# Optimization experiments

Measured on AMD Instinct MI355X. Metric: run time of the kernel, lower is better.

The kernel has to match this reference:

```python
import jax, jax.numpy as jnp
import numpy as np
from jax import lax

B, N, C, D = 8, 512, 37, 2048          # frames, rois/frame, classes (incl. bg), feat dim
SCORE_THR = 0.1
NMS_THR = 0.4
BBOX_STDS = np.array([0.1, 0.1, 0.2, 0.2], dtype=np.float32)


def setup_inputs() -> dict:
    key = jax.random.key(0)
    k1, k2, k3, k4, k5, k6 = jax.random.split(key, 6)
    # rois: [batch_idx, x1, y1, x2, y2] in a 600x1000 image
    x1 = jax.random.uniform(k1, (B, N)) * 900.0
    y1 = jax.random.uniform(k2, (B, N)) * 500.0
    w = jax.random.uniform(k3, (B, N)) * 120.0 + 8.0
    h = jax.random.uniform(k4, (B, N)) * 120.0 + 8.0
    bidx = jnp.broadcast_to(jnp.arange(B, dtype=jnp.float32)[:, None], (B, N))
    rois = jnp.stack([bidx, x1, y1, x1 + w, y1 + h], axis=-1)  # [B,N,5]
    bbox_pred = jax.random.normal(k5, (B, N, 4 * C)) * 0.5
    scores = jax.nn.softmax(jax.random.normal(k6, (B, N, C)) * 2.0, axis=-1)
    im_info = jnp.tile(jnp.array([[600.0, 1000.0, 1.0]], dtype=jnp.float32), (B, 1))
    roi_features = jax.random.normal(jax.random.fold_in(key, 7), (B, N, D))
    return {"rois": rois, "bbox_pred": bbox_pred, "scores": scores,
            "im_info": im_info, "roi_features": roi_features}


def _iou_matrix(b):
    # b: [N,4] -> [N,N] pairwise IoU (torchvision nms convention, no +1)
    area = (b[:, 2] - b[:, 0]) * (b[:, 3] - b[:, 1])
    lt = jnp.maximum(b[:, None, :2], b[None, :, :2])
    rb = jnp.minimum(b[:, None, 2:], b[None, :, 2:])
    wh = jnp.clip(rb - lt, 0.0)
    inter = wh[..., 0] * wh[..., 1]
    return inter / (area[:, None] + area[None, :] - inter + 1e-9)


def _nms_one(boxes, scores):
    # boxes [N,4], scores [N] -> keep mask [N] (greedy NMS on score-thresholded boxes)
    n = boxes.shape[0]
    valid = scores > SCORE_THR
    order = jnp.argsort(-jnp.where(valid, scores, -jnp.inf))
    b = boxes[order]
    v = valid[order]
    iou = _iou_matrix(b)
    idx = jnp.arange(n)

    def body(i, keep):
        suppressed = jnp.any((iou[:, i] > NMS_THR) & keep & (idx < i))
        return keep.at[i].set(v[i] & ~suppressed)

    keep_sorted = lax.fori_loop(0, n, body, jnp.zeros(n, bool))
    return jnp.zeros(n, bool).at[order].set(keep_sorted)


def reference(rois, bbox_pred, scores, im_info, roi_features):
    stds = jnp.asarray(BBOX_STDS)
    deltas = bbox_pred.reshape(B, N, C, 4) * stds
    # bbox_transform_inv
    w = (rois[..., 3] - rois[..., 1])[..., None]             # [B,N,1]
    h = (rois[..., 4] - rois[..., 2])[..., None]
    cx = rois[..., 1][..., None] + 0.5 * w
    cy = rois[..., 2][..., None] + 0.5 * h
    px = deltas[..., 0] * w + cx
    py = deltas[..., 1] * h + cy
    pw = jnp.exp(deltas[..., 2]) * w
    ph = jnp.exp(deltas[..., 3]) * h
    x1 = px - 0.5 * pw
    y1 = py - 0.5 * ph
    x2 = px + 0.5 * pw
    y2 = py + 0.5 * ph
    # clip_boxes to image
    xmax = (im_info[:, 1] - 1.0)[:, None, None]
    ymax = (im_info[:, 0] - 1.0)[:, None, None]
    boxes = jnp.stack([jnp.clip(x1, 0.0, xmax), jnp.clip(y1, 0.0, ymax),
                       jnp.clip(x2, 0.0, xmax), jnp.clip(y2, 0.0, ymax)], axis=-1)  # [B,N,C,4]
    # foreground classes 1..C-1, class-major layout: [B,C-1,N,*]
    boxes_fg = jnp.moveaxis(boxes[:, :, 1:, :], 2, 1)        # [B,C-1,N,4]
    scores_fg = jnp.moveaxis(scores[:, :, 1:], 2, 1)         # [B,C-1,N]
    keep = jax.vmap(jax.vmap(_nms_one))(boxes_fg, scores_fg)  # [B,C-1,N] bool
    cls_dets = jnp.where(keep[..., None],
                         jnp.concatenate([boxes_fg, scores_fg[..., None]], axis=-1),
                         0.0)                                 # [B,C-1,N,5]
    kept_feats = jnp.where(jnp.any(keep, axis=1)[..., None], roi_features, 0.0)  # [B,N,D]
    return cls_dets, kept_feats, keep
```

## Files before the change

### kernel.cpp

```cpp
#include <hip/hip_runtime.h>
#include <math.h>

#define BATCH 8
#define BN    512
#define NC    37
#define NFG   36
#define FD    2048


__global__ __launch_bounds__(64) void nms_kernel(
    const float* __restrict__ rois,
    const float* __restrict__ bbox_pred,
    const float* __restrict__ scores,
    const float* __restrict__ im_info,
    float* __restrict__ cls_dets,
    float* __restrict__ keep_out)
{
    const int bc   = blockIdx.x;
    const int b    = bc / NFG;
    const int cc   = bc % NFG;
    const int c    = cc + 1;
    const int lane = threadIdx.x;

    __shared__ float sb[BN][4];
    __shared__ float sarea[BN];
    __shared__ float cscore[BN];
    __shared__ int   cn[BN];
    __shared__ float kflag[BN];
    __shared__ unsigned char srem[BN];

    const float xmax = im_info[b * 3 + 1] - 1.0f;
    const float ymax = im_info[b * 3 + 0] - 1.0f;
    const unsigned long long lmask_lt = (lane == 0) ? 0ull : ((1ull << lane) - 1ull);

    float  sc[8];
    float4 bp[8];
    float  rx1[8], ry1[8], rx2[8], ry2[8];
#pragma unroll
    for (int r = 0; r < 8; ++r) {
        const int n = r * 64 + lane;
        sc[r] = scores[(size_t)(b * BN + n) * NC + c];
        bp[r] = *(const float4*)(bbox_pred + (size_t)(b * BN + n) * (4 * NC) + 4 * c);
        const float* rr = rois + (size_t)(b * BN + n) * 5;
        rx1[r] = rr[1]; ry1[r] = rr[2]; rx2[r] = rr[3]; ry2[r] = rr[4];
        kflag[n] = 0.0f;
    }

#pragma unroll
    for (int r = 0; r < 8; ++r) {
        const int n = r * 64 + lane;
        const float w  = rx2[r] - rx1[r];
        const float h  = ry2[r] - ry1[r];
        const float cx = rx1[r] + 0.5f * w;
        const float cy = ry1[r] + 0.5f * h;
        const float px = (bp[r].x * 0.1f) * w + cx;
        const float py = (bp[r].y * 0.1f) * h + cy;
        const float pw = expf(bp[r].z * 0.2f) * w;
        const float ph = expf(bp[r].w * 0.2f) * h;
        const float bx1 = fminf(fmaxf(px - 0.5f * pw, 0.0f), xmax);
        const float by1 = fminf(fmaxf(py - 0.5f * ph, 0.0f), ymax);
        const float bx2 = fminf(fmaxf(px + 0.5f * pw, 0.0f), xmax);
        const float by2 = fminf(fmaxf(py + 0.5f * ph, 0.0f), ymax);
        sb[n][0] = bx1; sb[n][1] = by1; sb[n][2] = bx2; sb[n][3] = by2;
        sarea[n] = (bx2 - bx1) * (by2 - by1);
    }

    int base = 0;
#pragma unroll
    for (int r = 0; r < 8; ++r) {
        const int n = r * 64 + lane;
        const bool valid = sc[r] > 0.1f;
        const unsigned long long m = __ballot(valid);
        if (valid) {
            const int pos = base + __popcll(m & lmask_lt);
            cscore[pos] = sc[r];
            cn[pos] = n;
        }
        base += __popcll(m);
    }
    const int V = base;
    __syncthreads();

    if (V <= 64) {
        float key; int id;
        if (lane < V) { key = cscore[lane]; id = cn[lane]; }
        else          { key = -INFINITY;    id = BN + lane; }
#pragma unroll
        for (int k = 2; k <= 64; k <<= 1) {
#pragma unroll
            for (int j = k >> 1; j > 0; j >>= 1) {
                const float ok = __shfl_xor(key, j);
                const int   oi = __shfl_xor(id, j);
                const bool is_lower   = (lane & j) == 0;
                const bool dir_desc   = (lane & k) == 0;
                const bool mine_first = (key > ok) || (key == ok && id < oi);
                bool take = mine_first ^ is_lower;
                if (!dir_desc) take = !take;
                if (take) { key = ok; id = oi; }
            }
        }
        float x1 = 0, y1 = 0, x2 = 0, y2 = 0, ar = 0;
        if (lane < V) { x1 = sb[id][0]; y1 = sb[id][1]; x2 = sb[id][2]; y2 = sb[id][3]; ar = sarea[id]; }
        unsigned long long rem = (V == 64) ? ~0ull : ((1ull << V) - 1ull);
        for (int i = 0; i < V; ++i) {
            if (!((rem >> i) & 1ull)) continue;
            const float ax1 = __shfl(x1, i);
            const float ay1 = __shfl(y1, i);
            const float ax2 = __shfl(x2, i);
            const float ay2 = __shfl(y2, i);
            const float aar = __shfl(ar, i);
            const float ix1 = fmaxf(ax1, x1);
            const float iy1 = fmaxf(ay1, y1);
            const float ix2 = fminf(ax2, x2);
            const float iy2 = fminf(ay2, y2);
            const float iw = fmaxf(ix2 - ix1, 0.0f);
            const float ih = fmaxf(iy2 - iy1, 0.0f);
            const float inter = iw * ih;
            const float iou = inter / (aar + ar - inter + 1e-9f);
            const unsigned long long sup = __ballot((iou > 0.4f) && (lane > i));
            rem &= ~sup;
        }
        if (lane < V && ((rem >> lane) & 1ull)) {
            kflag[id] = key;
        }
    } else {
        int P = 64; while (P < V) P <<= 1;
        for (int i = lane; i < P; i += 64) {
            if (i >= V) { cscore[i] = -INFINITY; cn[i] = BN + i; }
            srem[i] = (i < V) ? 1 : 0;
        }
        __syncthreads();
        for (int k = 2; k <= P; k <<= 1) {
            for (int j = k >> 1; j > 0; j >>= 1) {
                __syncthreads();
                for (int i = lane; i < P; i += 64) {
                    const int ixj = i ^ j;
                    if (ixj > i) {
                        const float ka = cscore[i], kb = cscore[ixj];
                        const int   ia = cn[i],     ib = cn[ixj];
                        const bool a_first = (ka > kb) || (ka == kb && ia < ib);
                        const bool up = ((i & k) == 0);
                        if (up ? !a_first : a_first) {
                            cscore[i] = kb; cscore[ixj] = ka;
                            cn[i] = ib;     cn[ixj] = ia;
                        }
                    }
                }
            }
        }
        __syncthreads();
        for (int i = 0; i < V; ++i) {
            __syncthreads();
            if (!srem[i]) continue;
            const int   ni  = cn[i];
            const float ax1 = sb[ni][0], ay1 = sb[ni][1];
            const float ax2 = sb[ni][2], ay2 = sb[ni][3];
            const float aar = sarea[ni];
            for (int jj = lane; jj < V; jj += 64) {
                if (jj > i && srem[jj]) {
                    const int nj = cn[jj];
                    const float ix1 = fmaxf(ax1, sb[nj][0]);
                    const float iy1 = fmaxf(ay1, sb[nj][1]);
                    const float ix2 = fminf(ax2, sb[nj][2]);
                    const float iy2 = fminf(ay2, sb[nj][3]);
                    const float iw = fmaxf(ix2 - ix1, 0.0f);
                    const float ih = fmaxf(iy2 - iy1, 0.0f);
                    const float inter = iw * ih;
                    const float iou = inter / (aar + sarea[nj] - inter + 1e-9f);
                    if (iou > 0.4f) srem[jj] = 0;
                }
            }
        }
        __syncthreads();
        for (int i = lane; i < V; i += 64) {
            if (srem[i]) kflag[cn[i]] = cscore[i];
        }
    }
    __syncthreads();

    const size_t rowbase = (size_t)(b * NFG + cc) * BN;
#pragma unroll
    for (int r = 0; r < 8; ++r) {
        const int n = r * 64 + lane;
        const float s = kflag[n];
        const bool kept = s > 0.0f;
        keep_out[rowbase + n] = kept ? 1.0f : 0.0f;
        float* cd = cls_dets + (rowbase + n) * 5;
        cd[0] = kept ? sb[n][0] : 0.0f;
        cd[1] = kept ? sb[n][1] : 0.0f;
        cd[2] = kept ? sb[n][2] : 0.0f;
        cd[3] = kept ? sb[n][3] : 0.0f;
        cd[4] = kept ? s : 0.0f;
    }
}

__global__ __launch_bounds__(256) void feat_kernel(
    const float* __restrict__ feats,
    const float* __restrict__ keepf,
    float* __restrict__ out_feats)
{
    const int bn = blockIdx.x;
    const int b  = bn >> 9;
    const int n  = bn & (BN - 1);

    __shared__ int s_any;
    if (threadIdx.x == 0) s_any = 0;
    __syncthreads();
    if (threadIdx.x < NFG) {
        if (keepf[((size_t)b * NFG + threadIdx.x) * BN + n] != 0.0f)
            s_any = 1;
    }
    __syncthreads();

    const float4* src = (const float4*)(feats + (size_t)bn * FD);
    float4*       dst = (float4*)(out_feats + (size_t)bn * FD);
    if (s_any) {
#pragma unroll
        for (int t = threadIdx.x; t < FD / 4; t += 256) dst[t] = src[t];
    } else {
        const float4 z = make_float4(0.f, 0.f, 0.f, 0.f);
#pragma unroll
        for (int t = threadIdx.x; t < FD / 4; t += 256) dst[t] = z;
    }
}

extern "C" void kernel_launch(void* const* d_in, const int* in_sizes, int n_in,
                              void* d_out, int out_size, void* d_ws, size_t ws_size,
                              hipStream_t stream) {
    const float* rois      = (const float*)d_in[0];
    const float* bbox_pred = (const float*)d_in[1];
    const float* scores    = (const float*)d_in[2];
    const float* im_info   = (const float*)d_in[3];
    const float* feats     = (const float*)d_in[4];

    float* out        = (float*)d_out;
    float* cls_dets   = out;
    float* kept_feats = out + (size_t)BATCH * NFG * BN * 5;
    float* keep_out   = kept_feats + (size_t)BATCH * BN * FD;

    nms_kernel<<<BATCH * NFG, 64, 0, stream>>>(rois, bbox_pred, scores, im_info,
                                               cls_dets, keep_out);
    feat_kernel<<<BATCH * BN, 256, 0, stream>>>(feats, keep_out, kept_feats);
}
```

Measured before the change: 109.2 us.

## Pack two NMS problems per block, precompute IoU masks, transpose keep flags

Each block now runs two independent (batch, class) NMS problems, one per wavefront, and replaces block barriers with wave barriers and per-wave shared buffers. The small-V path first computes a full per-lane suppression bitmask without early exits, then resolves it with a cheap ballot loop, which takes the shuffles and division off the serial dependency chain. The NMS kernel also writes a transposed byte keep map to workspace so the feature kernel checks 36 flags with nine 32-bit loads instead of 36 strided float reads. The trade-offs are doing every IoU even for already-suppressed boxes, an extra global write, and reliance on wave-local shared-memory ordering.

```diff
diff --git a/kernel.cpp b/kernel.cpp
--- a/kernel.cpp
+++ b/kernel.cpp
@@ -6,28 +6,31 @@
 #define NC    37
 #define NFG   36
 #define FD    2048
-
-
-__global__ __launch_bounds__(64) void nms_kernel(
+#define NW    2
+
+
+__global__ __launch_bounds__(128) void nms_kernel(
     const float* __restrict__ rois,
     const float* __restrict__ bbox_pred,
     const float* __restrict__ scores,
     const float* __restrict__ im_info,
     float* __restrict__ cls_dets,
-    float* __restrict__ keep_out)
+    float* __restrict__ keep_out,
+    unsigned char* __restrict__ keep_t)
 {
-    const int bc   = blockIdx.x;
+    const int wid  = threadIdx.x >> 6;
+    const int lane = threadIdx.x & 63;
+    const int bc   = blockIdx.x * NW + wid;
     const int b    = bc / NFG;
     const int cc   = bc % NFG;
     const int c    = cc + 1;
-    const int lane = threadIdx.x;
-
-    __shared__ float sb[BN][4];
-    __shared__ float sarea[BN];
-    __shared__ float cscore[BN];
-    __shared__ int   cn[BN];
-    __shared__ float kflag[BN];
-    __shared__ unsigned char srem[BN];
+
+    __shared__ float sb[NW][BN][4];
+    __shared__ float sarea[NW][BN];
+    __shared__ float cscore[NW][BN];
+    __shared__ int   cn[NW][BN];
+    __shared__ float kflag[NW][BN];
+    __shared__ unsigned char srem[NW][BN];
 
     const float xmax = im_info[b * 3 + 1] - 1.0f;
     const float ymax = im_info[b * 3 + 0] - 1.0f;
@@ -43,7 +46,7 @@
         bp[r] = *(const float4*)(bbox_pred + (size_t)(b * BN + n) * (4 * NC) + 4 * c);
         const float* rr = rois + (size_t)(b * BN + n) * 5;
         rx1[r] = rr[1]; ry1[r] = rr[2]; rx2[r] = rr[3]; ry2[r] = rr[4];
-        kflag[n] = 0.0f;
+        kflag[wid][n] = 0.0f;
     }
 
 #pragma unroll
@@ -61,8 +64,9 @@
         const float by1 = fminf(fmaxf(py - 0.5f * ph, 0.0f), ymax);
         const float bx2 = fminf(fmaxf(px + 0.5f * pw, 0.0f), xmax);
         const float by2 = fminf(fmaxf(py + 0.5f * ph, 0.0f), ymax);
-        sb[n][0] = bx1; sb[n][1] = by1; sb[n][2] = bx2; sb[n][3] = by2;
-        sarea[n] = (bx2 - bx1) * (by2 - by1);
+        sb[wid][n][0] = bx1; sb[wid][n][1] = by1;
+        sb[wid][n][2] = bx2; sb[wid][n][3] = by2;
+        sarea[wid][n] = (bx2 - bx1) * (by2 - by1);
     }
 
     int base = 0;
@@ -73,18 +77,18 @@
         const unsigned long long m = __ballot(valid);
         if (valid) {
             const int pos = base + __popcll(m & lmask_lt);
-            cscore[pos] = sc[r];
-            cn[pos] = n;
+            cscore[wid][pos] = sc[r];
+            cn[wid][pos] = n;
         }
         base += __popcll(m);
     }
     const int V = base;
-    __syncthreads();
+    __builtin_amdgcn_wave_barrier();
 
     if (V <= 64) {
         float key; int id;
-        if (lane < V) { key = cscore[lane]; id = cn[lane]; }
-        else          { key = -INFINITY;    id = BN + lane; }
+        if (lane < V) { key = cscore[wid][lane]; id = cn[wid][lane]; }
+        else          { key = -INFINITY;         id = BN + lane; }
 #pragma unroll
         for (int k = 2; k <= 64; k <<= 1) {
 #pragma unroll
@@ -100,10 +104,13 @@
             }
         }
         float x1 = 0, y1 = 0, x2 = 0, y2 = 0, ar = 0;
-        if (lane < V) { x1 = sb[id][0]; y1 = sb[id][1]; x2 = sb[id][2]; y2 = sb[id][3]; ar = sarea[id]; }
-        unsigned long long rem = (V == 64) ? ~0ull : ((1ull << V) - 1ull);
+        if (lane < V) {
+            x1 = sb[wid][id][0]; y1 = sb[wid][id][1];
+            x2 = sb[wid][id][2]; y2 = sb[wid][id][3];
+            ar = sarea[wid][id];
+        }
+        unsigned long long colmask = 0;
         for (int i = 0; i < V; ++i) {
-            if (!((rem >> i) & 1ull)) continue;
             const float ax1 = __shfl(x1, i);
             const float ay1 = __shfl(y1, i);
             const float ax2 = __shfl(x2, i);
@@ -117,98 +124,102 @@
             const float ih = fmaxf(iy2 - iy1, 0.0f);
             const float inter = iw * ih;
             const float iou = inter / (aar + ar - inter + 1e-9f);
-            const unsigned long long sup = __ballot((iou > 0.4f) && (lane > i));
-            rem &= ~sup;
+            if ((iou > 0.4f) && (i < lane)) colmask |= (1ull << i);
+        }
+        unsigned long long rem = (V == 64) ? ~0ull : ((1ull << V) - 1ull);
+        for (int i = 0; i < V; ++i) {
+            if (!((rem >> i) & 1ull)) continue;
+            rem &= ~__ballot((colmask >> i) & 1ull);
         }
         if (lane < V && ((rem >> lane) & 1ull)) {
-            kflag[id] = key;
+            kflag[wid][id] = key;
         }
     } else {
         int P = 64; while (P < V) P <<= 1;
         for (int i = lane; i < P; i += 64) {
-            if (i >= V) { cscore[i] = -INFINITY; cn[i] = BN + i; }
-            srem[i] = (i < V) ? 1 : 0;
-        }
-        __syncthreads();
+            if (i >= V) { cscore[wid][i] = -INFINITY; cn[wid][i] = BN + i; }
+            srem[wid][i] = (i < V) ? 1 : 0;
+        }
+        __builtin_amdgcn_wave_barrier();
         for (int k = 2; k <= P; k <<= 1) {
             for (int j = k >> 1; j > 0; j >>= 1) {
-                __syncthreads();
+                __builtin_amdgcn_wave_barrier();
                 for (int i = lane; i < P; i += 64) {
                     const int ixj = i ^ j;
                     if (ixj > i) {
-                        const float ka = cscore[i], kb = cscore[ixj];
-                        const int   ia = cn[i],     ib = cn[ixj];
+                        const float ka = cscore[wid][i], kb = cscore[wid][ixj];
+                        const int   ia = cn[wid][i],     ib = cn[wid][ixj];
                         const bool a_first = (ka > kb) || (ka == kb && ia < ib);
                         const bool up = ((i & k) == 0);
                         if (up ? !a_first : a_first) {
-                            cscore[i] = kb; cscore[ixj] = ka;
-                            cn[i] = ib;     cn[ixj] = ia;
+                            cscore[wid][i] = kb; cscore[wid][ixj] = ka;
+                            cn[wid][i] = ib;     cn[wid][ixj] = ia;
                         }
                     }
                 }
             }
         }
-        __syncthreads();
+        __builtin_amdgcn_wave_barrier();
         for (int i = 0; i < V; ++i) {
-            __syncthreads();
-            if (!srem[i]) continue;
-            const int   ni  = cn[i];
-            const float ax1 = sb[ni][0], ay1 = sb[ni][1];
-            const float ax2 = sb[ni][2], ay2 = sb[ni][3];
-            const float aar = sarea[ni];
+            __builtin_amdgcn_wave_barrier();
+            if (!srem[wid][i]) continue;
+            const int   ni  = cn[wid][i];
+            const float ax1 = sb[wid][ni][0], ay1 = sb[wid][ni][1];
+            const float ax2 = sb[wid][ni][2], ay2 = sb[wid][ni][3];
+            const float aar = sarea[wid][ni];
             for (int jj = lane; jj < V; jj += 64) {
-                if (jj > i && srem[jj]) {
-                    const int nj = cn[jj];
-                    const float ix1 = fmaxf(ax1, sb[nj][0]);
-                    const float iy1 = fmaxf(ay1, sb[nj][1]);
-                    const float ix2 = fminf(ax2, sb[nj][2]);
-                    const float iy2 = fminf(ay2, sb[nj][3]);
+                if (jj > i && srem[wid][jj]) {
+                    const int nj = cn[wid][jj];
+                    const float ix1 = fmaxf(ax1, sb[wid][nj][0]);
+                    const float iy1 = fmaxf(ay1, sb[wid][nj][1]);
+                    const float ix2 = fminf(ax2, sb[wid][nj][2]);
+                    const float iy2 = fminf(ay2, sb[wid][nj][3]);
                     const float iw = fmaxf(ix2 - ix1, 0.0f);
                     const float ih = fmaxf(iy2 - iy1, 0.0f);
                     const float inter = iw * ih;
-                    const float iou = inter / (aar + sarea[nj] - inter + 1e-9f);
-                    if (iou > 0.4f) srem[jj] = 0;
+                    const float iou = inter / (aar + sarea[wid][nj] - inter + 1e-9f);
+                    if (iou > 0.4f) srem[wid][jj] = 0;
                 }
             }
         }
-        __syncthreads();
+        __builtin_amdgcn_wave_barrier();
         for (int i = lane; i < V; i += 64) {
-            if (srem[i]) kflag[cn[i]] = cscore[i];
-        }
-    }
-    __syncthreads();
+            if (srem[wid][i]) kflag[wid][cn[wid][i]] = cscore[wid][i];
+        }
+    }
+    __builtin_amdgcn_wave_barrier();
 
     const size_t rowbase = (size_t)(b * NFG + cc) * BN;
 #pragma unroll
     for (int r = 0; r < 8; ++r) {
         const int n = r * 64 + lane;
-        const float s = kflag[n];
+        const float s = kflag[wid][n];
         const bool kept = s > 0.0f;
         keep_out[rowbase + n] = kept ? 1.0f : 0.0f;
+        keep_t[(size_t)(b * BN + n) * NFG + cc] = kept ? 1 : 0;
         float* cd = cls_dets + (rowbase + n) * 5;
-        cd[0] = kept ? sb[n][0] : 0.0f;
-        cd[1] = kept ? sb[n][1] : 0.0f;
-        cd[2] = kept ? sb[n][2] : 0.0f;
-        cd[3] = kept ? sb[n][3] : 0.0f;
+        cd[0] = kept ? sb[wid][n][0] : 0.0f;
+        cd[1] = kept ? sb[wid][n][1] : 0.0f;
+        cd[2] = kept ? sb[wid][n][2] : 0.0f;
+        cd[3] = kept ? sb[wid][n][3] : 0.0f;
         cd[4] = kept ? s : 0.0f;
     }
 }
 
 __global__ __launch_bounds__(256) void feat_kernel(
     const float* __restrict__ feats,
-    const float* __restrict__ keepf,
+    const unsigned char* __restrict__ keep_t,
     float* __restrict__ out_feats)
 {
     const int bn = blockIdx.x;
-    const int b  = bn >> 9;
-    const int n  = bn & (BN - 1);
 
     __shared__ int s_any;
     if (threadIdx.x == 0) s_any = 0;
     __syncthreads();
-    if (threadIdx.x < NFG) {
-        if (keepf[((size_t)b * NFG + threadIdx.x) * BN + n] != 0.0f)
-            s_any = 1;
+    if (threadIdx.x < 9) {
+        const unsigned int w = *(const unsigned int*)(keep_t + (size_t)bn * NFG
+                                                      + 4 * threadIdx.x);
+        if (w != 0u) s_any = 1;
     }
     __syncthreads();
 
@@ -238,7 +249,9 @@
     float* kept_feats = out + (size_t)BATCH * NFG * BN * 5;
     float* keep_out   = kept_feats + (size_t)BATCH * BN * FD;
 
-    nms_kernel<<<BATCH * NFG, 64, 0, stream>>>(rois, bbox_pred, scores, im_info,
-                                               cls_dets, keep_out);
-    feat_kernel<<<BATCH * BN, 256, 0, stream>>>(feats, keep_out, kept_feats);
+    unsigned char* keep_t = (unsigned char*)d_ws;
+
+    nms_kernel<<<(BATCH * NFG) / NW, 64 * NW, 0, stream>>>(
+        rois, bbox_pred, scores, im_info, cls_dets, keep_out, keep_t);
+    feat_kernel<<<BATCH * BN, 256, 0, stream>>>(feats, keep_t, kept_feats);
 }
```

Measured after the change: 109.0 us. Within noise of the previous version (-0.2%).
